# Kernel optimization log

Measured on AMD Instinct MI355X. Metric: run time of the kernel, lower is better.

Reference implementation:

```python
import jax, jax.numpy as jnp
import numpy as np

N_NODES = 50000
DROP_P = 0.2


def gcn_conv(x, edge_index, W, b):
    """PyG GCNConv: add self-loops, symmetric D^-1/2 (A+I) D^-1/2 normalization."""
    n = x.shape[0]
    loop = jnp.arange(n, dtype=edge_index.dtype)
    src = jnp.concatenate([edge_index[0], loop])  # [E+N]
    dst = jnp.concatenate([edge_index[1], loop])  # [E+N]
    # degree over destination (incl. self loop), all edge weights = 1
    deg = jax.ops.segment_sum(jnp.ones_like(src, dtype=x.dtype), dst, num_segments=n)
    dinv = jnp.where(deg > 0, jax.lax.rsqrt(deg), 0.0)
    norm = dinv[src] * dinv[dst]  # [E+N]
    h = x @ W  # [N, F_out] transform first (PyG order)
    msg = h[src] * norm[:, None]  # gather + scale
    out = jax.ops.segment_sum(msg, dst, num_segments=n)  # scatter-add
    return out + b


def setup_inputs() -> dict:
    key = jax.random.key(0)
    ks = jax.random.split(key, 4)
    x = jax.random.normal(ks[0], (N_NODES, 512), dtype=jnp.float32)
    edge_index = jax.random.randint(ks[1], (2, 800000), 0, N_NODES, dtype=jnp.int64)
    W1 = jax.random.normal(ks[2], (512, 256), dtype=jnp.float32) * (1.0 / np.sqrt(512))
    b1 = jnp.zeros((256,), dtype=jnp.float32)
    W2 = jax.random.normal(ks[3], (256, 128), dtype=jnp.float32) * (1.0 / np.sqrt(256))
    b2 = jnp.zeros((128,), dtype=jnp.float32)
    return {"x": x, "edge_index": edge_index, "W1": W1, "b1": b1, "W2": W2, "b2": b2}


def reference(x, edge_index, W1, b1, W2, b2):
    h = gcn_conv(x, edge_index, W1, b1)
    h = jax.nn.relu(h)
    # F.dropout(p=0.2) with training=True default; deterministic fixed-key mask
    keep = jax.random.bernoulli(jax.random.key(42), 1.0 - DROP_P, h.shape)
    h = jnp.where(keep, h / (1.0 - DROP_P), 0.0)
    h = gcn_conv(h, edge_index, W2, b2)
    return jax.nn.softmax(h, axis=1)
```

## Files before the change

### kernel.cpp

```cpp
#include <hip/hip_runtime.h>
#include <stdint.h>

#define N_NODES 50000
#define N_EDGES 800000
#define F0 512
#define F1 256
#define F2 128
#define CAP 64

typedef __attribute__((ext_vector_type(8))) short short8;
typedef __attribute__((ext_vector_type(4))) float float4v;

__device__ __forceinline__ uint32_t r8_rotl(uint32_t x, int r) {
    return (x << r) | (x >> (32 - r));
}

__device__ __forceinline__ uint32_t r8_bits32(uint32_t idx) {
    const uint32_t ks0 = 0u;
    const uint32_t ks1 = 42u;
    const uint32_t ks2 = 0x1BD11BDAu ^ ks0 ^ ks1;
    uint32_t x0 = ks0;
    uint32_t x1 = idx + ks1;
#define R8R(r) { x0 += x1; x1 = r8_rotl(x1, (r)); x1 ^= x0; }
    R8R(13) R8R(15) R8R(26) R8R(6)
    x0 += ks1; x1 += ks2 + 1u;
    R8R(17) R8R(29) R8R(16) R8R(24)
    x0 += ks2; x1 += ks0 + 2u;
    R8R(13) R8R(15) R8R(26) R8R(6)
    x0 += ks0; x1 += ks1 + 3u;
    R8R(17) R8R(29) R8R(16) R8R(24)
    x0 += ks1; x1 += ks2 + 4u;
    R8R(13) R8R(15) R8R(26) R8R(6)
    x0 += ks2; x1 += ks0 + 5u;
#undef R8R
    return x0 ^ x1;
}

__device__ __forceinline__ int r8_keep(uint32_t idx) {
    return (r8_bits32(idx) >> 9) < 0x666667u;
}

__device__ __forceinline__ unsigned short r8_f2bf(float f) {
    uint32_t u = __float_as_uint(f);
    uint32_t r = u + 0x7fffu + ((u >> 16) & 1u);
    return (unsigned short)(r >> 16);
}

__device__ __forceinline__ void r8_lds_barrier() {
    asm volatile("s_waitcnt lgkmcnt(0)\n\ts_barrier" ::: "memory");
}

__global__ void r8_zero(int* __restrict__ p, int n) {
    int i = blockIdx.x * 256 + threadIdx.x;
    if (i < n) p[i] = 0;
}

__global__ void r8_detect(const uint32_t* __restrict__ ei, int* __restrict__ flag) {
    int t = threadIdx.x;
    uint32_t v = ei[2 * t + 1] | ei[128 + 2 * t + 1];
    unsigned long long any_nonzero = __ballot(v != 0u);
    if (t == 0) flag[0] = (any_nonzero == 0ull) ? 1 : 0;
}

__global__ void r8_fill(const int* __restrict__ ei, const int* __restrict__ flag,
                        int* __restrict__ cursor, int* __restrict__ bucket) {
    int e = blockIdx.x * 256 + threadIdx.x;
    if (e < N_EDGES) {
        int f = flag[0];
        int s = ei[(size_t)e << f];
        int d = ei[(size_t)(N_EDGES + e) << f];
        int pos = atomicAdd(&cursor[d], 1);
        if (pos < CAP) bucket[(size_t)d * CAP + pos] = s;
    }
}

__global__ void r8_dinv(const int* __restrict__ cursor, float* __restrict__ dinv) {
    int v = blockIdx.x * 256 + threadIdx.x;
    if (v < N_NODES) dinv[v] = 1.0f / sqrtf((float)(cursor[v] + 1));
}

__global__ __launch_bounds__(256)
void r8_mask(unsigned char* __restrict__ mask) {
    int i = blockIdx.x * 256 + threadIdx.x;
    if (i < N_NODES * 64) {
        uint32_t b = (uint32_t)i * 4u;
        unsigned m = (unsigned)r8_keep(b) | ((unsigned)r8_keep(b + 1) << 1) |
                     ((unsigned)r8_keep(b + 2) << 2) | ((unsigned)r8_keep(b + 3) << 3);
        mask[i] = (unsigned char)m;
    }
}

__global__ void r8_w1t(const float* __restrict__ W1, unsigned short* __restrict__ Bt) {
    int k = blockIdx.x;
    int n = threadIdx.x;
    Bt[(size_t)n * F0 + k] = r8_f2bf(W1[(size_t)k * F1 + n]);
}

__global__ void r8_w2t(const float* __restrict__ W2, unsigned short* __restrict__ Bt) {
    int k = blockIdx.x;
    int n = threadIdx.x;
    Bt[(size_t)n * F1 + k] = r8_f2bf(W2[(size_t)k * F2 + n]);
}

#define G1_LDA 40
__global__ __launch_bounds__(256)
void r8_gemm1(const float* __restrict__ A, const unsigned short* __restrict__ Bt,
              unsigned short* __restrict__ C, int M) {
    __shared__ unsigned short As[2][128][G1_LDA];
    __shared__ unsigned short Bs[2][128][G1_LDA];
    const int bn = blockIdx.x * 128;
    const int bm = blockIdx.y * 128;
    const int tid = threadIdx.x;
    const int wave = tid >> 6;
    const int lane = tid & 63;
    const int wm = (wave & 1) * 64;
    const int wn = (wave >> 1) * 64;
    const int l15 = lane & 15;
    const int quad = lane >> 4;

    const int sr = tid >> 1;
    const int sk = (tid & 1) * 16;

    float4v acc[4][4];
#pragma unroll
    for (int i = 0; i < 4; ++i)
#pragma unroll
        for (int j = 0; j < 4; ++j) acc[i][j] = (float4v){0.f, 0.f, 0.f, 0.f};

    const int arow = bm + sr;
    const bool avalid = arow < M;
    const float* aptr = A + (size_t)(avalid ? arow : 0) * F0 + sk;
    const unsigned short* bptr = Bt + (size_t)(bn + sr) * F0 + sk;

    float4 apfA[4], apfB[4];
    short8 bpfA[2], bpfB[2];
#pragma unroll
    for (int q = 0; q < 4; ++q) {
        apfA[q] = make_float4(0.f, 0.f, 0.f, 0.f);
        apfB[q] = make_float4(0.f, 0.f, 0.f, 0.f);
    }

    auto load_tile = [&](int kt, float4 (&apf)[4], short8 (&bpf)[2]) {
        const int k0 = kt * 32;
        if (avalid) {
            const float4* ap = (const float4*)(aptr + k0);
#pragma unroll
            for (int q = 0; q < 4; ++q) apf[q] = ap[q];
        }
        bpf[0] = *(const short8*)(bptr + k0);
        bpf[1] = *(const short8*)(bptr + k0 + 8);
    };

    auto write_buf = [&](int buf, const float4 (&apf)[4], const short8 (&bpf)[2]) {
        union { short8 v[2]; unsigned short u[16]; } at;
#pragma unroll
        for (int q = 0; q < 4; ++q) {
            at.u[q * 4 + 0] = r8_f2bf(apf[q].x);
            at.u[q * 4 + 1] = r8_f2bf(apf[q].y);
            at.u[q * 4 + 2] = r8_f2bf(apf[q].z);
            at.u[q * 4 + 3] = r8_f2bf(apf[q].w);
        }
        *(short8*)&As[buf][sr][sk] = at.v[0];
        *(short8*)&As[buf][sr][sk + 8] = at.v[1];
        *(short8*)&Bs[buf][sr][sk] = bpf[0];
        *(short8*)&Bs[buf][sr][sk + 8] = bpf[1];
    };

    auto compute = [&](int cur) {
        short8 afr[4], bfr[4];
#pragma unroll
        for (int mi = 0; mi < 4; ++mi)
            afr[mi] = *(const short8*)&As[cur][wm + mi * 16 + l15][quad * 8];
#pragma unroll
        for (int ni = 0; ni < 4; ++ni)
            bfr[ni] = *(const short8*)&Bs[cur][wn + ni * 16 + l15][quad * 8];
#pragma unroll
        for (int mi = 0; mi < 4; ++mi)
#pragma unroll
            for (int ni = 0; ni < 4; ++ni)
                acc[mi][ni] = __builtin_amdgcn_mfma_f32_16x16x32_bf16(
                    afr[mi], bfr[ni], acc[mi][ni], 0, 0, 0);
    };

    const int NT = F0 / 32;
    load_tile(0, apfA, bpfA);
    write_buf(0, apfA, bpfA);
    load_tile(1, apfB, bpfB);
    r8_lds_barrier();

    for (int kt = 0; kt < NT; kt += 2) {
        if (kt + 2 < NT) load_tile(kt + 2, apfA, bpfA);
        compute(0);
        write_buf(1, apfB, bpfB);
        r8_lds_barrier();
        if (kt + 3 < NT) load_tile(kt + 3, apfB, bpfB);
        compute(1);
        if (kt + 2 < NT) write_buf(0, apfA, bpfA);
        r8_lds_barrier();
    }

#pragma unroll
    for (int mi = 0; mi < 4; ++mi) {
#pragma unroll
        for (int r = 0; r < 4; ++r) {
            int row = bm + wm + mi * 16 + quad * 4 + r;
            if (row < M) {
                unsigned short* cp = C + (size_t)row * F1 + bn + wn + l15;
#pragma unroll
                for (int ni = 0; ni < 4; ++ni) cp[ni * 16] = r8_f2bf(acc[mi][ni][r]);
            }
        }
    }
}

#define G2_LDA 40
__global__ __launch_bounds__(256)
void r8_gemm2(const unsigned short* __restrict__ A, const unsigned short* __restrict__ Bt,
              unsigned short* __restrict__ C, int M) {
    __shared__ unsigned short As[2][64][G2_LDA];
    __shared__ unsigned short Bs[2][128][G2_LDA];
    const int bm = blockIdx.x * 64;
    const int tid = threadIdx.x;
    const int wave = tid >> 6;
    const int lane = tid & 63;
    const int wm = (wave & 1) * 32;
    const int wn = (wave >> 1) * 64;
    const int l15 = lane & 15;
    const int quad = lane >> 4;

    const int asr = tid >> 2;
    const int ask = (tid & 3) * 8;
    const int bsr = tid >> 1;
    const int bsk = (tid & 1) * 16;

    float4v acc[2][4];
#pragma unroll
    for (int i = 0; i < 2; ++i)
#pragma unroll
        for (int j = 0; j < 4; ++j) acc[i][j] = (float4v){0.f, 0.f, 0.f, 0.f};

    const int arow = bm + asr;
    const bool avalid = arow < M;
    const unsigned short* aptr = A + (size_t)(avalid ? arow : 0) * F1 + ask;
    const unsigned short* bptr = Bt + (size_t)bsr * F1 + bsk;

    short8 apfA = (short8){0,0,0,0,0,0,0,0}, apfB = (short8){0,0,0,0,0,0,0,0};
    short8 bpfA[2], bpfB[2];

    auto load_tile = [&](int kt, short8& apf, short8 (&bpf)[2]) {
        const int k0 = kt * 32;
        if (avalid) apf = *(const short8*)(aptr + k0);
        bpf[0] = *(const short8*)(bptr + k0);
        bpf[1] = *(const short8*)(bptr + k0 + 8);
    };

    auto write_buf = [&](int buf, const short8& apf, const short8 (&bpf)[2]) {
        *(short8*)&As[buf][asr][ask] = apf;
        *(short8*)&Bs[buf][bsr][bsk] = bpf[0];
        *(short8*)&Bs[buf][bsr][bsk + 8] = bpf[1];
    };

    auto compute = [&](int cur) {
        short8 afr[2], bfr[4];
#pragma unroll
        for (int mi = 0; mi < 2; ++mi)
            afr[mi] = *(const short8*)&As[cur][wm + mi * 16 + l15][quad * 8];
#pragma unroll
        for (int ni = 0; ni < 4; ++ni)
            bfr[ni] = *(const short8*)&Bs[cur][wn + ni * 16 + l15][quad * 8];
#pragma unroll
        for (int mi = 0; mi < 2; ++mi)
#pragma unroll
            for (int ni = 0; ni < 4; ++ni)
                acc[mi][ni] = __builtin_amdgcn_mfma_f32_16x16x32_bf16(
                    afr[mi], bfr[ni], acc[mi][ni], 0, 0, 0);
    };

    const int NT = F1 / 32;
    load_tile(0, apfA, bpfA);
    write_buf(0, apfA, bpfA);
    load_tile(1, apfB, bpfB);
    r8_lds_barrier();

    for (int kt = 0; kt < NT; kt += 2) {
        if (kt + 2 < NT) load_tile(kt + 2, apfA, bpfA);
        compute(0);
        write_buf(1, apfB, bpfB);
        r8_lds_barrier();
        if (kt + 3 < NT) load_tile(kt + 3, apfB, bpfB);
        compute(1);
        if (kt + 2 < NT) write_buf(0, apfA, bpfA);
        r8_lds_barrier();
    }

#pragma unroll
    for (int mi = 0; mi < 2; ++mi) {
#pragma unroll
        for (int r = 0; r < 4; ++r) {
            int row = bm + wm + mi * 16 + quad * 4 + r;
            if (row < M) {
                unsigned short* cp = C + (size_t)row * F2 + wn + l15;
#pragma unroll
                for (int ni = 0; ni < 4; ++ni) cp[ni * 16] = r8_f2bf(acc[mi][ni][r]);
            }
        }
    }
}

__global__ __launch_bounds__(256)
void r8_prop1(const unsigned short* __restrict__ h1, const int* __restrict__ bucket,
              const int* __restrict__ deg, const float* __restrict__ dinv,
              const float* __restrict__ b1, const unsigned char* __restrict__ mask,
              unsigned short* __restrict__ a1) {
    const int v = (blockIdx.x << 2) + (threadIdx.x >> 6);
    const int lane = threadIdx.x & 63;
    const float dv = dinv[v];
    int cnt = deg[v]; if (cnt > CAP) cnt = CAP;

    int s_l = 0; float w_l = 0.f;
    if (lane < cnt) {
        s_l = bucket[(size_t)v * CAP + lane];
        w_l = dinv[s_l] * dv;
    }

    const unsigned short* hrow = h1 + (size_t)lane * 4;
    uint2 hq = *(const uint2*)(h1 + (size_t)v * F1 + lane * 4);
    const float w0 = dv * dv;
    float ax = __uint_as_float(hq.x << 16) * w0;
    float ay = __uint_as_float(hq.x & 0xffff0000u) * w0;
    float az = __uint_as_float(hq.y << 16) * w0;
    float aw = __uint_as_float(hq.y & 0xffff0000u) * w0;

    for (int j = 0; j < cnt; j += 8) {
        int   s[8];
        float w[8];
#pragma unroll
        for (int u = 0; u < 8; ++u) {
            s[u] = __shfl(s_l, j + u);
            w[u] = __shfl(w_l, j + u);
        }
        uint2 r[8];
#pragma unroll
        for (int u = 0; u < 8; ++u)
            r[u] = *(const uint2*)(hrow + (size_t)s[u] * F1);
#pragma unroll
        for (int u = 0; u < 8; ++u) {
            ax += __uint_as_float(r[u].x << 16) * w[u];
            ay += __uint_as_float(r[u].x & 0xffff0000u) * w[u];
            az += __uint_as_float(r[u].y << 16) * w[u];
            aw += __uint_as_float(r[u].y & 0xffff0000u) * w[u];
        }
    }

    float4 bb = *(const float4*)(b1 + lane * 4);
    ax = fmaxf(ax + bb.x, 0.f);
    ay = fmaxf(ay + bb.y, 0.f);
    az = fmaxf(az + bb.z, 0.f);
    aw = fmaxf(aw + bb.w, 0.f);
    unsigned m = mask[(size_t)v * 64 + lane];
    ax = (m & 1u) ? ax * 1.25f : 0.0f;
    ay = (m & 2u) ? ay * 1.25f : 0.0f;
    az = (m & 4u) ? az * 1.25f : 0.0f;
    aw = (m & 8u) ? aw * 1.25f : 0.0f;
    uint2 st;
    st.x = (uint32_t)r8_f2bf(ax) | ((uint32_t)r8_f2bf(ay) << 16);
    st.y = (uint32_t)r8_f2bf(az) | ((uint32_t)r8_f2bf(aw) << 16);
    *(uint2*)(a1 + (size_t)v * F1 + lane * 4) = st;
}

__global__ __launch_bounds__(256)
void r8_prop2(const unsigned short* __restrict__ h2, const int* __restrict__ bucket,
              const int* __restrict__ deg, const float* __restrict__ dinv,
              const float* __restrict__ b2, float* __restrict__ out) {
    const int v = (blockIdx.x << 2) + (threadIdx.x >> 6);
    const int lane = threadIdx.x & 63;
    const float dv = dinv[v];
    int cnt = deg[v]; if (cnt > CAP) cnt = CAP;

    int s_l = 0; float w_l = 0.f;
    if (lane < cnt) {
        s_l = bucket[(size_t)v * CAP + lane];
        w_l = dinv[s_l] * dv;
    }

    const unsigned short* hrow = h2 + (size_t)lane * 2;
    uint32_t hq = *(const uint32_t*)(h2 + (size_t)v * F2 + lane * 2);
    const float w0 = dv * dv;
    float ax = __uint_as_float(hq << 16) * w0;
    float ay = __uint_as_float(hq & 0xffff0000u) * w0;

    for (int j = 0; j < cnt; j += 8) {
        int   s[8];
        float w[8];
#pragma unroll
        for (int u = 0; u < 8; ++u) {
            s[u] = __shfl(s_l, j + u);
            w[u] = __shfl(w_l, j + u);
        }
        uint32_t r[8];
#pragma unroll
        for (int u = 0; u < 8; ++u)
            r[u] = *(const uint32_t*)(hrow + (size_t)s[u] * F2);
#pragma unroll
        for (int u = 0; u < 8; ++u) {
            ax += __uint_as_float(r[u] << 16) * w[u];
            ay += __uint_as_float(r[u] & 0xffff0000u) * w[u];
        }
    }

    float2 bb = *(const float2*)(b2 + lane * 2);
    ax += bb.x; ay += bb.y;
    float m = fmaxf(ax, ay);
#pragma unroll
    for (int o = 32; o >= 1; o >>= 1) m = fmaxf(m, __shfl_xor(m, o, 64));
    float ex = expf(ax - m), ey = expf(ay - m);
    float s = ex + ey;
#pragma unroll
    for (int o = 32; o >= 1; o >>= 1) s += __shfl_xor(s, o, 64);
    float inv = 1.0f / s;
    *(float2*)(out + (size_t)v * F2 + lane * 2) = make_float2(ex * inv, ey * inv);
}

extern "C" void kernel_launch(void* const* d_in, const int* in_sizes, int n_in,
                              void* d_out, int out_size, void* d_ws, size_t ws_size,
                              hipStream_t stream) {
    const float* x  = (const float*)d_in[0];
    const int*   ei = (const int*)d_in[1];
    const float* W1 = (const float*)d_in[2];
    const float* b1 = (const float*)d_in[3];
    const float* W2 = (const float*)d_in[4];
    const float* b2 = (const float*)d_in[5];
    float* out = (float*)d_out;

    char* ws = (char*)d_ws;
    size_t o = 0;
    auto alloc = [&](size_t bytes) -> char* {
        char* p = ws + o;
        o += (bytes + 511) & ~(size_t)511;
        return p;
    };
    int*            flag   = (int*)           alloc(4);
    int*            cursor = (int*)           alloc((size_t)N_NODES * 4);
    float*          dinv   = (float*)         alloc((size_t)N_NODES * 4);
    int*            bucket = (int*)           alloc((size_t)N_NODES * CAP * 4);
    unsigned char*  maskp  = (unsigned char*) alloc((size_t)N_NODES * 64);
    unsigned short* w1t    = (unsigned short*)alloc((size_t)F1 * F0 * 2);
    unsigned short* w2t    = (unsigned short*)alloc((size_t)F2 * F1 * 2);
    unsigned short* h1     = (unsigned short*)alloc((size_t)N_NODES * F1 * 2);
    unsigned short* a1     = (unsigned short*)alloc((size_t)N_NODES * F1 * 2);
    unsigned short* h2     = (unsigned short*)alloc((size_t)N_NODES * F2 * 2);

    r8_zero<<<(N_NODES + 255) / 256, 256, 0, stream>>>(cursor, N_NODES);
    r8_detect<<<1, 64, 0, stream>>>((const uint32_t*)ei, flag);
    r8_fill<<<(N_EDGES + 255) / 256, 256, 0, stream>>>(ei, flag, cursor, bucket);
    r8_dinv<<<(N_NODES + 255) / 256, 256, 0, stream>>>(cursor, dinv);
    r8_mask<<<(N_NODES * 64 + 255) / 256, 256, 0, stream>>>(maskp);
    r8_w1t<<<F0, F1, 0, stream>>>(W1, w1t);
    r8_w2t<<<F1, F2, 0, stream>>>(W2, w2t);

    dim3 g1(F1 / 128, (N_NODES + 127) / 128);
    r8_gemm1<<<g1, 256, 0, stream>>>(x, w1t, h1, N_NODES);

    r8_prop1<<<N_NODES / 4, 256, 0, stream>>>(h1, bucket, cursor, dinv, b1, maskp, a1);

    r8_gemm2<<<(N_NODES + 63) / 64, 256, 0, stream>>>(a1, w2t, h2, N_NODES);

    r8_prop2<<<N_NODES / 4, 256, 0, stream>>>(h2, bucket, cursor, dinv, b2, out);
}
```

Baseline: 371.7 us.

## Drop LDS staging in both GEMMs and load MFMA fragments directly from global memory

Both dense transforms stop staging A and B tiles through double-buffered shared memory with barriers. Each lane now loads its MFMA fragments straight from global memory, converting fp32 A to bf16 in registers for gemm1. This removes LDS traffic and barrier stalls, but data is no longer shared across waves, so global/L2 traffic rises and loads are less coalesced. Out-of-range rows are clamped to the last row instead of being zero-filled.

```diff
diff --git a/kernel.cpp b/kernel.cpp
--- a/kernel.cpp
+++ b/kernel.cpp
@@ -46,10 +46,6 @@
     return (unsigned short)(r >> 16);
 }
 
-__device__ __forceinline__ void r8_lds_barrier() {
-    asm volatile("s_waitcnt lgkmcnt(0)\n\ts_barrier" ::: "memory");
-}
-
 __global__ void r8_zero(int* __restrict__ p, int n) {
     int i = blockIdx.x * 256 + threadIdx.x;
     if (i < n) p[i] = 0;
@@ -102,12 +98,9 @@
     Bt[(size_t)n * F1 + k] = r8_f2bf(W2[(size_t)k * F2 + n]);
 }
 
-#define G1_LDA 40
 __global__ __launch_bounds__(256)
 void r8_gemm1(const float* __restrict__ A, const unsigned short* __restrict__ Bt,
               unsigned short* __restrict__ C, int M) {
-    __shared__ unsigned short As[2][128][G1_LDA];
-    __shared__ unsigned short Bs[2][128][G1_LDA];
     const int bn = blockIdx.x * 128;
     const int bm = blockIdx.y * 128;
     const int tid = threadIdx.x;
@@ -118,85 +111,47 @@
     const int l15 = lane & 15;
     const int quad = lane >> 4;
 
-    const int sr = tid >> 1;
-    const int sk = (tid & 1) * 16;
-
     float4v acc[4][4];
 #pragma unroll
     for (int i = 0; i < 4; ++i)
 #pragma unroll
         for (int j = 0; j < 4; ++j) acc[i][j] = (float4v){0.f, 0.f, 0.f, 0.f};
 
-    const int arow = bm + sr;
-    const bool avalid = arow < M;
-    const float* aptr = A + (size_t)(avalid ? arow : 0) * F0 + sk;
-    const unsigned short* bptr = Bt + (size_t)(bn + sr) * F0 + sk;
-
-    float4 apfA[4], apfB[4];
-    short8 bpfA[2], bpfB[2];
-#pragma unroll
-    for (int q = 0; q < 4; ++q) {
-        apfA[q] = make_float4(0.f, 0.f, 0.f, 0.f);
-        apfB[q] = make_float4(0.f, 0.f, 0.f, 0.f);
-    }
-
-    auto load_tile = [&](int kt, float4 (&apf)[4], short8 (&bpf)[2]) {
-        const int k0 = kt * 32;
-        if (avalid) {
-            const float4* ap = (const float4*)(aptr + k0);
-#pragma unroll
-            for (int q = 0; q < 4; ++q) apf[q] = ap[q];
-        }
-        bpf[0] = *(const short8*)(bptr + k0);
-        bpf[1] = *(const short8*)(bptr + k0 + 8);
-    };
-
-    auto write_buf = [&](int buf, const float4 (&apf)[4], const short8 (&bpf)[2]) {
-        union { short8 v[2]; unsigned short u[16]; } at;
-#pragma unroll
-        for (int q = 0; q < 4; ++q) {
-            at.u[q * 4 + 0] = r8_f2bf(apf[q].x);
-            at.u[q * 4 + 1] = r8_f2bf(apf[q].y);
-            at.u[q * 4 + 2] = r8_f2bf(apf[q].z);
-            at.u[q * 4 + 3] = r8_f2bf(apf[q].w);
-        }
-        *(short8*)&As[buf][sr][sk] = at.v[0];
-        *(short8*)&As[buf][sr][sk + 8] = at.v[1];
-        *(short8*)&Bs[buf][sr][sk] = bpf[0];
-        *(short8*)&Bs[buf][sr][sk + 8] = bpf[1];
-    };
-
-    auto compute = [&](int cur) {
+    const float* ap[4];
+#pragma unroll
+    for (int mi = 0; mi < 4; ++mi) {
+        int r = bm + wm + mi * 16 + l15;
+        if (r > M - 1) r = M - 1;
+        ap[mi] = A + (size_t)r * F0 + quad * 8;
+    }
+    const unsigned short* bp[4];
+#pragma unroll
+    for (int ni = 0; ni < 4; ++ni)
+        bp[ni] = Bt + (size_t)(bn + wn + ni * 16 + l15) * F0 + quad * 8;
+
+#pragma unroll 4
+    for (int k0 = 0; k0 < F0; k0 += 32) {
         short8 afr[4], bfr[4];
 #pragma unroll
-        for (int mi = 0; mi < 4; ++mi)
-            afr[mi] = *(const short8*)&As[cur][wm + mi * 16 + l15][quad * 8];
+        for (int mi = 0; mi < 4; ++mi) {
+            float4 f0 = *(const float4*)(ap[mi] + k0);
+            float4 f1 = *(const float4*)(ap[mi] + k0 + 4);
+            union { short8 v; unsigned short u[8]; } t;
+            t.u[0] = r8_f2bf(f0.x); t.u[1] = r8_f2bf(f0.y);
+            t.u[2] = r8_f2bf(f0.z); t.u[3] = r8_f2bf(f0.w);
+            t.u[4] = r8_f2bf(f1.x); t.u[5] = r8_f2bf(f1.y);
+            t.u[6] = r8_f2bf(f1.z); t.u[7] = r8_f2bf(f1.w);
+            afr[mi] = t.v;
+        }
 #pragma unroll
         for (int ni = 0; ni < 4; ++ni)
-            bfr[ni] = *(const short8*)&Bs[cur][wn + ni * 16 + l15][quad * 8];
+            bfr[ni] = *(const short8*)(bp[ni] + k0);
 #pragma unroll
         for (int mi = 0; mi < 4; ++mi)
 #pragma unroll
             for (int ni = 0; ni < 4; ++ni)
                 acc[mi][ni] = __builtin_amdgcn_mfma_f32_16x16x32_bf16(
                     afr[mi], bfr[ni], acc[mi][ni], 0, 0, 0);
-    };
-
-    const int NT = F0 / 32;
-    load_tile(0, apfA, bpfA);
-    write_buf(0, apfA, bpfA);
-    load_tile(1, apfB, bpfB);
-    r8_lds_barrier();
-
-    for (int kt = 0; kt < NT; kt += 2) {
-        if (kt + 2 < NT) load_tile(kt + 2, apfA, bpfA);
-        compute(0);
-        write_buf(1, apfB, bpfB);
-        r8_lds_barrier();
-        if (kt + 3 < NT) load_tile(kt + 3, apfB, bpfB);
-        compute(1);
-        if (kt + 2 < NT) write_buf(0, apfA, bpfA);
-        r8_lds_barrier();
     }
 
 #pragma unroll
@@ -213,12 +168,9 @@
     }
 }
 
-#define G2_LDA 40
 __global__ __launch_bounds__(256)
 void r8_gemm2(const unsigned short* __restrict__ A, const unsigned short* __restrict__ Bt,
               unsigned short* __restrict__ C, int M) {
-    __shared__ unsigned short As[2][64][G2_LDA];
-    __shared__ unsigned short Bs[2][128][G2_LDA];
     const int bm = blockIdx.x * 64;
     const int tid = threadIdx.x;
     const int wave = tid >> 6;
@@ -228,69 +180,39 @@
     const int l15 = lane & 15;
     const int quad = lane >> 4;
 
-    const int asr = tid >> 2;
-    const int ask = (tid & 3) * 8;
-    const int bsr = tid >> 1;
-    const int bsk = (tid & 1) * 16;
-
     float4v acc[2][4];
 #pragma unroll
     for (int i = 0; i < 2; ++i)
 #pragma unroll
         for (int j = 0; j < 4; ++j) acc[i][j] = (float4v){0.f, 0.f, 0.f, 0.f};
 
-    const int arow = bm + asr;
-    const bool avalid = arow < M;
-    const unsigned short* aptr = A + (size_t)(avalid ? arow : 0) * F1 + ask;
-    const unsigned short* bptr = Bt + (size_t)bsr * F1 + bsk;
-
-    short8 apfA = (short8){0,0,0,0,0,0,0,0}, apfB = (short8){0,0,0,0,0,0,0,0};
-    short8 bpfA[2], bpfB[2];
-
-    auto load_tile = [&](int kt, short8& apf, short8 (&bpf)[2]) {
-        const int k0 = kt * 32;
-        if (avalid) apf = *(const short8*)(aptr + k0);
-        bpf[0] = *(const short8*)(bptr + k0);
-        bpf[1] = *(const short8*)(bptr + k0 + 8);
-    };
-
-    auto write_buf = [&](int buf, const short8& apf, const short8 (&bpf)[2]) {
-        *(short8*)&As[buf][asr][ask] = apf;
-        *(short8*)&Bs[buf][bsr][bsk] = bpf[0];
-        *(short8*)&Bs[buf][bsr][bsk + 8] = bpf[1];
-    };
-
-    auto compute = [&](int cur) {
+    const unsigned short* ap[2];
+#pragma unroll
+    for (int mi = 0; mi < 2; ++mi) {
+        int r = bm + wm + mi * 16 + l15;
+        if (r > M - 1) r = M - 1;
+        ap[mi] = A + (size_t)r * F1 + quad * 8;
+    }
+    const unsigned short* bp[4];
+#pragma unroll
+    for (int ni = 0; ni < 4; ++ni)
+        bp[ni] = Bt + (size_t)(wn + ni * 16 + l15) * F1 + quad * 8;
+
+#pragma unroll 4
+    for (int k0 = 0; k0 < F1; k0 += 32) {
         short8 afr[2], bfr[4];
 #pragma unroll
         for (int mi = 0; mi < 2; ++mi)
-            afr[mi] = *(const short8*)&As[cur][wm + mi * 16 + l15][quad * 8];
+            afr[mi] = *(const short8*)(ap[mi] + k0);
 #pragma unroll
         for (int ni = 0; ni < 4; ++ni)
-            bfr[ni] = *(const short8*)&Bs[cur][wn + ni * 16 + l15][quad * 8];
+            bfr[ni] = *(const short8*)(bp[ni] + k0);
 #pragma unroll
         for (int mi = 0; mi < 2; ++mi)
 #pragma unroll
             for (int ni = 0; ni < 4; ++ni)
                 acc[mi][ni] = __builtin_amdgcn_mfma_f32_16x16x32_bf16(
                     afr[mi], bfr[ni], acc[mi][ni], 0, 0, 0);
-    };
-
-    const int NT = F1 / 32;
-    load_tile(0, apfA, bpfA);
-    write_buf(0, apfA, bpfA);
-    load_tile(1, apfB, bpfB);
-    r8_lds_barrier();
-
-    for (int kt = 0; kt < NT; kt += 2) {
-        if (kt + 2 < NT) load_tile(kt + 2, apfA, bpfA);
-        compute(0);
-        write_buf(1, apfB, bpfB);
-        r8_lds_barrier();
-        if (kt + 3 < NT) load_tile(kt + 3, apfB, bpfB);
-        compute(1);
-        if (kt + 2 < NT) write_buf(0, apfA, bpfA);
-        r8_lds_barrier();
     }
 
 #pragma unroll
```

Result: slower. 426.8 us (+14.8%).
